# Optimization experiments

Hardware: AMD Instinct MI355X
Metric: run time of the kernel (lower is better)

Reference implementation:

```python
import jax, jax.numpy as jnp
import numpy as np

N, INC, INN = 8, 32, 50000
OUTC, OUTN, D = 64, 8192, 32  # D = uniform neighbor count (maxD)


def setup_inputs() -> dict:
    key = jax.random.key(0)
    k1, k2, k3, k4, k5 = jax.random.split(key, 5)
    x = jax.random.normal(k1, (N, INC, INN), dtype=jnp.float32)
    nf_weight = jax.random.normal(k2, (INC, INN), dtype=jnp.float32)
    # torch init: uniform(-1,1) * sqrt(6/(1+5*inc)); exact distribution irrelevant for correctness baseline
    ft_weight = (jax.random.uniform(k3, (INC, OUTC), dtype=jnp.float32) * 2.0 - 1.0) * np.sqrt(6.0 / (1.0 + 5 * INC)).astype(np.float32)
    bias = 0.2 * jax.random.normal(k4, (OUTC, OUTN), dtype=jnp.float32)
    A = jax.random.randint(k5, (OUTN, D), 0, INN, dtype=jnp.int32)
    return {"x": x, "nf_weight": nf_weight, "ft_weight": ft_weight, "bias": bias, "A": A}


def reference(x, nf_weight, ft_weight, bias, A):
    # op_order '132': (1) node/feature weight on input, (3) gather+max reduce, (2) feature transform
    y = x * nf_weight                      # (N, inc, inn)
    gathered = y[:, :, A]                  # (N, inc, outn, D) -- padded adjacency gather
    red = jnp.max(gathered, axis=-1)       # (N, inc, outn)    -- reduction='max', mask all-ones (uniform degree)
    out = jnp.einsum('nio,ik->nko', red, ft_weight)  # (N, outc, outn)
    return out + bias                      # bias (outc, outn) broadcast over N
```

## Files before the change

### kernel.cpp

```cpp
#include <hip/hip_runtime.h>
#include <math.h>

#define NN   8
#define INCH 32
#define INN  50000
#define OUTC 64
#define OUTN 8192
#define DD   32
#define CC   256
#define NPL  8
#define PLDW ((size_t)INN * 16)

typedef unsigned short ushortT;

__device__ __forceinline__ unsigned f2bf_u(float f) {
  unsigned u = __float_as_uint(f);
  return (u + 0x7FFFu + ((u >> 16) & 1u)) >> 16;
}


__global__ __launch_bounds__(256) void prep_kernel(
    const float* __restrict__ x, const float* __restrict__ nf, unsigned* __restrict__ yTc) {
  __shared__ float tile[CC][33];
  const int t = threadIdx.x;
  const int j0 = blockIdx.x * 32;
  const int jmax = min(32, INN - j0);

  const int q  = t & 7;
  const int r0 = t >> 3;

  if (q * 4 < jmax) {
    const float4 nv = *(const float4*)(nf + (size_t)r0 * INN + j0 + 4 * q);
    #pragma unroll
    for (int p = 0; p < 8; ++p) {
      const int c = (p << 5) + r0;
      const float4 xv = *(const float4*)(x + (size_t)c * INN + j0 + 4 * q);
      float4 pr;
      pr.x = xv.x * nv.x; pr.y = xv.y * nv.y; pr.z = xv.z * nv.z; pr.w = xv.w * nv.w;
      *(float4*)&tile[c][4 * q] = pr;
    }
  }
  __syncthreads();

  const int lane = t & 63;
  const int wave = t >> 6;
  #pragma unroll
  for (int r = 0; r < 8; ++r) {
    const int jl = wave * 8 + r;
    if (jl < jmax) {
      #pragma unroll
      for (int e = 0; e < 2; ++e) {
        const int clo = lane + 64 * e;
        const unsigned lo = f2bf_u(tile[clo][jl]);
        const unsigned hi = f2bf_u(tile[clo + 128][jl]);
        const int pl  = clo >> 4;
        const int pos = clo & 15;
        yTc[(size_t)pl * PLDW + (size_t)(j0 + jl) * 16 + pos] = lo | (hi << 16);
      }
    }
  }
}

__global__ __launch_bounds__(256) void gather_kernel(
    const unsigned* __restrict__ yTc, const int* __restrict__ A, unsigned* __restrict__ red32) {
  __shared__ int Al[64 * 33];
  const int t = threadIdx.x;
  const int lane = t & 63;
  const int wave = t >> 6;
  const int ck = blockIdx.x & 7;
  const int ob = blockIdx.x >> 3;
  const int o0 = ob * 64;

  #pragma unroll
  for (int k = 0; k < 8; ++k) {
    const int f = k * 256 + t;
    Al[(f >> 5) * 33 + (f & 31)] = A[(size_t)o0 * DD + f];
  }
  __syncthreads();

  const unsigned* plane = yTc + (size_t)ck * PLDW;
  const int osub = wave * 16 + (lane >> 2);
  const int cq   = lane & 3;

  float l0 = -INFINITY, l1 = -INFINITY, l2 = -INFINITY, l3 = -INFINITY;
  float h0 = -INFINITY, h1 = -INFINITY, h2 = -INFINITY, h3 = -INFINITY;

  #pragma unroll 8
  for (int d = 0; d < 32; ++d) {
    const int idx = Al[osub * 33 + d];
    const uint4 v = *(const uint4*)(plane + (size_t)idx * 16 + cq * 4);
    l0 = fmaxf(l0, __uint_as_float(v.x << 16));  h0 = fmaxf(h0, __uint_as_float(v.x & 0xffff0000u));
    l1 = fmaxf(l1, __uint_as_float(v.y << 16));  h1 = fmaxf(h1, __uint_as_float(v.y & 0xffff0000u));
    l2 = fmaxf(l2, __uint_as_float(v.z << 16));  h2 = fmaxf(h2, __uint_as_float(v.z & 0xffff0000u));
    l3 = fmaxf(l3, __uint_as_float(v.w << 16));  h3 = fmaxf(h3, __uint_as_float(v.w & 0xffff0000u));
  }

  uint4 pk;
  pk.x = (__float_as_uint(l0) >> 16) | (__float_as_uint(h0) & 0xffff0000u);
  pk.y = (__float_as_uint(l1) >> 16) | (__float_as_uint(h1) & 0xffff0000u);
  pk.z = (__float_as_uint(l2) >> 16) | (__float_as_uint(h2) & 0xffff0000u);
  pk.w = (__float_as_uint(l3) >> 16) | (__float_as_uint(h3) & 0xffff0000u);
  *(uint4*)(red32 + ((size_t)(o0 + osub) * 128) + ck * 16 + cq * 4) = pk;
}

__global__ __launch_bounds__(256) void out_kernel(
    const unsigned* __restrict__ red32, const float* __restrict__ ft,
    const float* __restrict__ bias, float* __restrict__ out) {
  __shared__ float rtile[64][65];
  __shared__ float ftl[32][64];
  const int t = threadIdx.x;
  const int lane = t & 63;
  const int wave = t >> 6;
  const int np = blockIdx.x >> 7;
  const int ot = blockIdx.x & 127;
  const int o0 = ot * 64;
  const int hi = np >> 1;
  const int sb = (np & 1) * 64;

  #pragma unroll
  for (int q = 0; q < 8; ++q) {
    const int idx = q * 256 + t;
    ftl[idx >> 6][idx & 63] = ft[idx];
  }
  #pragma unroll
  for (int i = 0; i < 2; ++i) {
    const int r = (t >> 3) + 32 * i;
    const int g = t & 7;
    const unsigned* src = red32 + (size_t)(o0 + r) * 128 + sb + g * 8;
    const uint4 v0 = *(const uint4*)(src);
    const uint4 v1 = *(const uint4*)(src + 4);
    const unsigned w[8] = {v0.x, v0.y, v0.z, v0.w, v1.x, v1.y, v1.z, v1.w};
    float* dst = &rtile[r][g * 8];
    #pragma unroll
    for (int u = 0; u < 8; ++u)
      dst[u] = __uint_as_float(hi ? (w[u] & 0xffff0000u) : (w[u] << 16));
  }
  __syncthreads();

  const int n  = np * 2 + (wave & 1);
  const int kh = (wave >> 1) * 32;
  const int cb = (wave & 1) * 32;

  float rv[32];
  #pragma unroll
  for (int i = 0; i < 32; ++i) rv[i] = rtile[lane][cb + i];

  float acc[32];
  #pragma unroll
  for (int kk = 0; kk < 32; ++kk) acc[kk] = 0.f;
  #pragma unroll
  for (int i = 0; i < 32; ++i) {
    #pragma unroll
    for (int kk = 0; kk < 32; ++kk)
      acc[kk] += rv[i] * ftl[i][kh + kk];
  }

  float* op = out + (size_t)n * OUTC * OUTN + o0 + lane;
  const float* bp = bias + o0 + lane;
  #pragma unroll
  for (int kk = 0; kk < 32; ++kk) {
    const int k = kh + kk;
    op[(size_t)k * OUTN] = acc[kk] + bp[(size_t)k * OUTN];
  }
}

extern "C" void kernel_launch(void* const* d_in, const int* in_sizes, int n_in,
                              void* d_out, int out_size, void* d_ws, size_t ws_size,
                              hipStream_t stream) {
  const float* x    = (const float*)d_in[0];
  const float* nf   = (const float*)d_in[1];
  const float* ft   = (const float*)d_in[2];
  const float* bias = (const float*)d_in[3];
  const int*   A    = (const int*)d_in[4];
  float* out = (float*)d_out;

  unsigned* yTc   = (unsigned*)d_ws;
  unsigned* red32 = (unsigned*)((char*)d_ws + NPL * PLDW * 4);

  hipLaunchKernelGGL(prep_kernel,   dim3((INN + 31) / 32),  dim3(256), 0, stream, x, nf, yTc);
  hipLaunchKernelGGL(gather_kernel, dim3((OUTN / 64) * NPL), dim3(256), 0, stream, yTc, A, red32);
  hipLaunchKernelGGL(out_kernel,    dim3(512),              dim3(256), 0, stream, red32, ft, bias, out);
}
```

Baseline: 47.09 us.

## Fuse gather and output kernels into one cooperative kernel with grid sync

Merges the gather-max kernel and the feature-transform/bias kernel into a single cooperative launch of 256 blocks of 512 threads, separated by a grid-wide barrier. Each block now handles several gather tiles and two output tiles in loops. The goal is to drop one kernel launch and its inter-kernel gap. In exchange it adds grid.sync cost, caps the grid at 256 blocks with less latency hiding for the random gathers, and puts more register pressure on the 512-thread blocks.

```diff
diff --git a/kernel.cpp b/kernel.cpp
--- a/kernel.cpp
+++ b/kernel.cpp
@@ -1,5 +1,8 @@
 #include <hip/hip_runtime.h>
+#include <hip/hip_cooperative_groups.h>
 #include <math.h>
+
+namespace cg = cooperative_groups;
 
 #define NN   8
 #define INCH 32
@@ -11,8 +14,6 @@
 #define NPL  8
 #define PLDW ((size_t)INN * 16)
 
-typedef unsigned short ushortT;
-
 __device__ __forceinline__ unsigned f2bf_u(float f) {
   unsigned u = __float_as_uint(f);
   return (u + 0x7FFFu + ((u >> 16) & 1u)) >> 16;
@@ -61,106 +62,117 @@
   }
 }
 
-__global__ __launch_bounds__(256) void gather_kernel(
-    const unsigned* __restrict__ yTc, const int* __restrict__ A, unsigned* __restrict__ red32) {
-  __shared__ int Al[64 * 33];
+__global__ __launch_bounds__(512) void go_kernel(
+    const unsigned* __restrict__ yTc, const int* __restrict__ A,
+    const float* __restrict__ ft, const float* __restrict__ bias,
+    unsigned* __restrict__ red32, float* __restrict__ out) {
+  __shared__ __align__(16) char smem[24832];
   const int t = threadIdx.x;
-  const int lane = t & 63;
-  const int wave = t >> 6;
-  const int ck = blockIdx.x & 7;
-  const int ob = blockIdx.x >> 3;
-  const int o0 = ob * 64;
-
-  #pragma unroll
-  for (int k = 0; k < 8; ++k) {
-    const int f = k * 256 + t;
-    Al[(f >> 5) * 33 + (f & 31)] = A[(size_t)o0 * DD + f];
-  }
-  __syncthreads();
-
-  const unsigned* plane = yTc + (size_t)ck * PLDW;
-  const int osub = wave * 16 + (lane >> 2);
-  const int cq   = lane & 3;
-
-  float l0 = -INFINITY, l1 = -INFINITY, l2 = -INFINITY, l3 = -INFINITY;
-  float h0 = -INFINITY, h1 = -INFINITY, h2 = -INFINITY, h3 = -INFINITY;
-
-  #pragma unroll 8
-  for (int d = 0; d < 32; ++d) {
-    const int idx = Al[osub * 33 + d];
-    const uint4 v = *(const uint4*)(plane + (size_t)idx * 16 + cq * 4);
-    l0 = fmaxf(l0, __uint_as_float(v.x << 16));  h0 = fmaxf(h0, __uint_as_float(v.x & 0xffff0000u));
-    l1 = fmaxf(l1, __uint_as_float(v.y << 16));  h1 = fmaxf(h1, __uint_as_float(v.y & 0xffff0000u));
-    l2 = fmaxf(l2, __uint_as_float(v.z << 16));  h2 = fmaxf(h2, __uint_as_float(v.z & 0xffff0000u));
-    l3 = fmaxf(l3, __uint_as_float(v.w << 16));  h3 = fmaxf(h3, __uint_as_float(v.w & 0xffff0000u));
-  }
-
-  uint4 pk;
-  pk.x = (__float_as_uint(l0) >> 16) | (__float_as_uint(h0) & 0xffff0000u);
-  pk.y = (__float_as_uint(l1) >> 16) | (__float_as_uint(h1) & 0xffff0000u);
-  pk.z = (__float_as_uint(l2) >> 16) | (__float_as_uint(h2) & 0xffff0000u);
-  pk.w = (__float_as_uint(l3) >> 16) | (__float_as_uint(h3) & 0xffff0000u);
-  *(uint4*)(red32 + ((size_t)(o0 + osub) * 128) + ck * 16 + cq * 4) = pk;
-}
-
-__global__ __launch_bounds__(256) void out_kernel(
-    const unsigned* __restrict__ red32, const float* __restrict__ ft,
-    const float* __restrict__ bias, float* __restrict__ out) {
-  __shared__ float rtile[64][65];
-  __shared__ float ftl[32][64];
-  const int t = threadIdx.x;
-  const int lane = t & 63;
-  const int wave = t >> 6;
-  const int np = blockIdx.x >> 7;
-  const int ot = blockIdx.x & 127;
-  const int o0 = ot * 64;
-  const int hi = np >> 1;
-  const int sb = (np & 1) * 64;
-
-  #pragma unroll
-  for (int q = 0; q < 8; ++q) {
-    const int idx = q * 256 + t;
-    ftl[idx >> 6][idx & 63] = ft[idx];
-  }
-  #pragma unroll
-  for (int i = 0; i < 2; ++i) {
-    const int r = (t >> 3) + 32 * i;
-    const int g = t & 7;
-    const unsigned* src = red32 + (size_t)(o0 + r) * 128 + sb + g * 8;
-    const uint4 v0 = *(const uint4*)(src);
-    const uint4 v1 = *(const uint4*)(src + 4);
-    const unsigned w[8] = {v0.x, v0.y, v0.z, v0.w, v1.x, v1.y, v1.z, v1.w};
-    float* dst = &rtile[r][g * 8];
+  const int b = blockIdx.x;
+  cg::grid_group grid = cg::this_grid();
+
+  {
+    int* Al = (int*)smem;
+    const int ck = b & 7;
+    const int ob = b >> 3;
+    const unsigned* plane = yTc + (size_t)ck * PLDW;
+    const int osub = t >> 2;
+    const int cq   = t & 3;
+
     #pragma unroll
-    for (int u = 0; u < 8; ++u)
-      dst[u] = __uint_as_float(hi ? (w[u] & 0xffff0000u) : (w[u] << 16));
-  }
-  __syncthreads();
-
-  const int n  = np * 2 + (wave & 1);
-  const int kh = (wave >> 1) * 32;
-  const int cb = (wave & 1) * 32;
-
-  float rv[32];
-  #pragma unroll
-  for (int i = 0; i < 32; ++i) rv[i] = rtile[lane][cb + i];
-
-  float acc[32];
-  #pragma unroll
-  for (int kk = 0; kk < 32; ++kk) acc[kk] = 0.f;
-  #pragma unroll
-  for (int i = 0; i < 32; ++i) {
+    for (int pp = 0; pp < 2; ++pp) {
+      const int o0 = ob * 256 + pp * 128;
+      #pragma unroll
+      for (int k = 0; k < 8; ++k) {
+        const int f = k * 512 + t;
+        Al[(f >> 5) * 33 + (f & 31)] = A[(size_t)o0 * DD + f];
+      }
+      __syncthreads();
+
+      float l0 = -INFINITY, l1 = -INFINITY, l2 = -INFINITY, l3 = -INFINITY;
+      float h0 = -INFINITY, h1 = -INFINITY, h2 = -INFINITY, h3 = -INFINITY;
+      #pragma unroll 8
+      for (int d = 0; d < 32; ++d) {
+        const int idx = Al[osub * 33 + d];
+        const uint4 v = *(const uint4*)(plane + (size_t)idx * 16 + cq * 4);
+        l0 = fmaxf(l0, __uint_as_float(v.x << 16));  h0 = fmaxf(h0, __uint_as_float(v.x & 0xffff0000u));
+        l1 = fmaxf(l1, __uint_as_float(v.y << 16));  h1 = fmaxf(h1, __uint_as_float(v.y & 0xffff0000u));
+        l2 = fmaxf(l2, __uint_as_float(v.z << 16));  h2 = fmaxf(h2, __uint_as_float(v.z & 0xffff0000u));
+        l3 = fmaxf(l3, __uint_as_float(v.w << 16));  h3 = fmaxf(h3, __uint_as_float(v.w & 0xffff0000u));
+      }
+      uint4 pk;
+      pk.x = (__float_as_uint(l0) >> 16) | (__float_as_uint(h0) & 0xffff0000u);
+      pk.y = (__float_as_uint(l1) >> 16) | (__float_as_uint(h1) & 0xffff0000u);
+      pk.z = (__float_as_uint(l2) >> 16) | (__float_as_uint(h2) & 0xffff0000u);
+      pk.w = (__float_as_uint(l3) >> 16) | (__float_as_uint(h3) & 0xffff0000u);
+      *(uint4*)(red32 + (size_t)(o0 + osub) * 128 + ck * 16 + cq * 4) = pk;
+      __syncthreads();
+    }
+  }
+
+  grid.sync();
+
+  {
+    float* rtile = (float*)smem;
+    float* ftl   = (float*)(smem + 64 * 65 * 4);
+    const int lane = t & 63;
+    const int wv   = t >> 6;
+
     #pragma unroll
-    for (int kk = 0; kk < 32; ++kk)
-      acc[kk] += rv[i] * ftl[i][kh + kk];
-  }
-
-  float* op = out + (size_t)n * OUTC * OUTN + o0 + lane;
-  const float* bp = bias + o0 + lane;
-  #pragma unroll
-  for (int kk = 0; kk < 32; ++kk) {
-    const int k = kh + kk;
-    op[(size_t)k * OUTN] = acc[kk] + bp[(size_t)k * OUTN];
+    for (int rep = 0; rep < 2; ++rep) {
+      const int tile = b + rep * 256;
+      const int np = tile >> 7;
+      const int ot = tile & 127;
+      const int o0 = ot * 64;
+      const int hi = np >> 1;
+      const int sb = (np & 1) * 64;
+
+      #pragma unroll
+      for (int q = 0; q < 4; ++q) {
+        const int idx = q * 512 + t;
+        ftl[idx] = ft[idx];
+      }
+      {
+        const int r = t >> 3;
+        const int g = t & 7;
+        const unsigned* src = red32 + (size_t)(o0 + r) * 128 + sb + g * 8;
+        const uint4 v0 = *(const uint4*)(src);
+        const uint4 v1 = *(const uint4*)(src + 4);
+        const unsigned w[8] = {v0.x, v0.y, v0.z, v0.w, v1.x, v1.y, v1.z, v1.w};
+        float* dst = &rtile[r * 65 + g * 8];
+        #pragma unroll
+        for (int u = 0; u < 8; ++u)
+          dst[u] = __uint_as_float(hi ? (w[u] & 0xffff0000u) : (w[u] << 16));
+      }
+      __syncthreads();
+
+      const int n  = np * 2 + (wv & 1);
+      const int kh = (wv >> 1) * 16;
+      const int cb = (wv & 1) * 32;
+
+      float rv[32];
+      #pragma unroll
+      for (int i = 0; i < 32; ++i) rv[i] = rtile[lane * 65 + cb + i];
+
+      float acc[16];
+      #pragma unroll
+      for (int kk = 0; kk < 16; ++kk) acc[kk] = 0.f;
+      #pragma unroll
+      for (int i = 0; i < 32; ++i) {
+        #pragma unroll
+        for (int kk = 0; kk < 16; ++kk)
+          acc[kk] += rv[i] * ftl[i * 64 + kh + kk];
+      }
+
+      float* op = out + (size_t)n * OUTC * OUTN + o0 + lane;
+      const float* bp = bias + o0 + lane;
+      #pragma unroll
+      for (int kk = 0; kk < 16; ++kk) {
+        const int k = kh + kk;
+        op[(size_t)k * OUTN] = acc[kk] + bp[(size_t)k * OUTN];
+      }
+      __syncthreads();
+    }
   }
 }
 
@@ -177,7 +189,12 @@
   unsigned* yTc   = (unsigned*)d_ws;
   unsigned* red32 = (unsigned*)((char*)d_ws + NPL * PLDW * 4);
 
-  hipLaunchKernelGGL(prep_kernel,   dim3((INN + 31) / 32),  dim3(256), 0, stream, x, nf, yTc);
-  hipLaunchKernelGGL(gather_kernel, dim3((OUTN / 64) * NPL), dim3(256), 0, stream, yTc, A, red32);
-  hipLaunchKernelGGL(out_kernel,    dim3(512),              dim3(256), 0, stream, red32, ft, bias, out);
-}
+  hipLaunchKernelGGL(prep_kernel, dim3((INN + 31) / 32), dim3(256), 0, stream, x, nf, yTc);
+
+  void* args[6];
+  const unsigned* yTc_a = yTc;  const int* A_a = A;  const float* ft_a = ft;
+  const float* bias_a = bias;   unsigned* red_a = red32;  float* out_a = out;
+  args[0] = (void*)&yTc_a;  args[1] = (void*)&A_a;   args[2] = (void*)&ft_a;
+  args[3] = (void*)&bias_a; args[4] = (void*)&red_a; args[5] = (void*)&out_a;
+  hipLaunchCooperativeKernel((void*)go_kernel, dim3(256), dim3(512), args, 0, stream);
+}
```

Measured after the change: 89.54 us. +90.1%, slower.
